# Kernel tuning notes

Measured on AMD Instinct MI355X. Metric: run time of the kernel, lower is better.

Reference implementation:

```python
import jax, jax.numpy as jnp
import numpy as np

B, T, D, N = 64, 32, 128, 128


def setup_inputs() -> dict:
    key = jax.random.key(0)
    ks = jax.random.split(key, 7)
    init_mu = 0.05
    ini_sigma = -4.6
    inp = {
        'x': jax.random.normal(ks[0], (B, T, D), dtype=jnp.float32),
        'U_z': init_mu * jax.random.normal(ks[1], (D, N), dtype=jnp.float32),
        'W_z': init_mu * jax.random.normal(ks[2], (N, N), dtype=jnp.float32),
        'U_r': init_mu * jax.random.normal(ks[3], (D, N), dtype=jnp.float32),
        'W_r': init_mu * jax.random.normal(ks[4], (N, N), dtype=jnp.float32),
        'U_h': init_mu * jax.random.normal(ks[5], (D, N), dtype=jnp.float32),
        'W_h': init_mu * jax.random.normal(ks[6], (N, N), dtype=jnp.float32),
        'uz_sigma': jnp.full((N,), ini_sigma, dtype=jnp.float32),
        'wz_sigma': jnp.full((N,), ini_sigma, dtype=jnp.float32),
        'ur_sigma': jnp.full((N,), ini_sigma, dtype=jnp.float32),
        'wr_sigma': jnp.full((N,), ini_sigma, dtype=jnp.float32),
        'uh_sigma': jnp.full((N,), ini_sigma, dtype=jnp.float32),
        'wh_sigma': jnp.full((N,), ini_sigma, dtype=jnp.float32),
    }
    return inp


def _outer(a, b):
    # [B,n] x [B,n] -> [B,n,n]
    return a[:, :, None] * b[:, None, :]


def _hadamard_sigma(s1, s2, m1, m2):
    # s1*s2 + diag(m1) s2 diag(m1) + diag(m2) s1 diag(m2)
    return s1 * s2 + _outer(m1, m1) * s2 + _outer(m2, m2) * s1


def reference(x, U_z, W_z, U_r, W_r, U_h, W_h,
              uz_sigma, wz_sigma, ur_sigma, wr_sigma, uh_sigma, wh_sigma):
    b, t, d = x.shape
    n = U_z.shape[1]
    idx = jnp.arange(n)
    sp = jax.nn.softplus
    dUz, dWz = jnp.diag(sp(uz_sigma)), jnp.diag(sp(wz_sigma))
    dUr, dWr = jnp.diag(sp(ur_sigma)), jnp.diag(sp(wr_sigma))
    dUh, dWh = jnp.diag(sp(uh_sigma)), jnp.diag(sp(wh_sigma))

    def step(carry, xt):
        mu_p, S_p = carry  # [B,n], [B,n,n]
        xx = jnp.sum(xt * xt, axis=1)[:, None, None]
        pp = jnp.sum(mu_p * mu_p, axis=1)[:, None, None]
        trS = jnp.trace(S_p, axis1=1, axis2=2)[:, None, None]

        def gate_cov(W, dW, dU):
            # W^T Sigma W + ||prev||^2 dW + tr(Sigma) dW + ||x||^2 dU
            S1 = jnp.einsum('ki,bkl,lj->bij', W, S_p, W)
            return S1 + pp * dW + trS * dW + xx * dU

        az = xt @ U_z + mu_p @ W_z
        z = jax.nn.sigmoid(az)
        gz = z * (1.0 - z)
        S_z = gate_cov(W_z, dWz, dUz) * _outer(gz, gz)

        ar = xt @ U_r + mu_p @ W_r
        r = jax.nn.sigmoid(ar)
        gr = r * (1.0 - r)
        S_r = gate_cov(W_r, dWr, dUr) * _outer(gr, gr)

        rh = mu_p * r
        ah = xt @ U_h + rh @ W_h
        h = jnp.tanh(ah)
        gh = 1.0 - h * h
        S_g = _hadamard_sigma(S_p, S_r, mu_p, r)
        rr = jnp.sum(rh * rh, axis=1)[:, None, None]
        trg = jnp.trace(S_g, axis1=1, axis2=2)[:, None, None]
        S_hh = jnp.einsum('ki,bkl,lj->bij', W_h, S_g, W_h) + rr * dWh + trg * dWh + xx * dUh
        S_h = S_hh * _outer(gh, gh)

        mu = z * mu_p + (1.0 - z) * h
        sa = _hadamard_sigma(S_z, S_p, z, mu_p)
        sb = _hadamard_sigma(S_z, S_h, 1.0 - z, h)
        S = sa + sb - S_z * _outer(mu_p, h) - S_z * _outer(h, mu_p)
        S = jnp.where(jnp.isfinite(S), S, jnp.zeros_like(S))
        S = S.at[:, idx, idx].set(jnp.abs(S[:, idx, idx]))
        return (mu, S), (mu, S)

    mu0 = jnp.zeros((b, n), dtype=x.dtype)
    S0 = jnp.zeros((b, n, n), dtype=x.dtype)
    _, (mu_seq, S_seq) = jax.lax.scan(step, (mu0, S0), jnp.swapaxes(x, 0, 1))
    # [B,T,n], [B,T,n,n]
    return jnp.swapaxes(mu_seq, 0, 1), jnp.swapaxes(S_seq, 0, 1)
```

## Files before the change

### kernel.cpp

```cpp
#include <hip/hip_runtime.h>
#include <math.h>

#define B_ 64
#define T_ 32
#define D_ 128
#define N_ 128
#define SBS 72
#define PTS 136

typedef __attribute__((ext_vector_type(8))) short s8v;
typedef __attribute__((ext_vector_type(4))) float f4;

__device__ __forceinline__ float softplus_f(float v){ return (v > 20.f) ? v : log1pf(expf(v)); }
__device__ __forceinline__ float sigmoid_f(float v){ return 1.f / (1.f + expf(-v)); }
__device__ __forceinline__ float wred(float v){
#pragma unroll
    for (int o = 32; o > 0; o >>= 1) v += __shfl_down(v, o, 64);
    return v;
}
__device__ __forceinline__ void split2(float v, unsigned short& h, unsigned short& l){
    unsigned int u  = __float_as_uint(v);
    unsigned int rh = u + 0x7fffu + ((u >> 16) & 1u);
    h = (unsigned short)(rh >> 16);
    float fh = __uint_as_float(rh & 0xffff0000u);
    float lo = v - fh;
    unsigned int ul = __float_as_uint(lo);
    unsigned int rl = ul + 0x7fffu + ((ul >> 16) & 1u);
    l = (unsigned short)(rl >> 16);
}
__device__ __forceinline__ void split4_store(float4 v, unsigned short* hp, unsigned short* lp){
    unsigned short h0,h1,h2,h3,l0,l1,l2,l3;
    split2(v.x,h0,l0); split2(v.y,h1,l1); split2(v.z,h2,l2); split2(v.w,h3,l3);
    uint2 H = make_uint2((unsigned)h0 | ((unsigned)h1 << 16), (unsigned)h2 | ((unsigned)h3 << 16));
    uint2 L = make_uint2((unsigned)l0 | ((unsigned)l1 << 16), (unsigned)l2 | ((unsigned)l3 << 16));
    *(uint2*)hp = H; *(uint2*)lp = L;
}
__device__ __forceinline__ f4 mfma3(s8v ah, s8v al, s8v bh, s8v bl, f4 c){
    c = __builtin_amdgcn_mfma_f32_16x16x32_bf16(ah, bh, c, 0, 0, 0);
    c = __builtin_amdgcn_mfma_f32_16x16x32_bf16(ah, bl, c, 0, 0, 0);
    c = __builtin_amdgcn_mfma_f32_16x16x32_bf16(al, bh, c, 0, 0, 0);
    return c;
}

__global__ __launch_bounds__(256)
void prep_w(const float* __restrict__ Wz, const float* __restrict__ Wr,
            const float* __restrict__ Wh, unsigned short* __restrict__ WT){
    int gate = blockIdx.x, n0 = blockIdx.y * 16, tid = threadIdx.x;
    const float* W = (gate == 0) ? Wz : (gate == 1) ? Wr : Wh;
    unsigned short* hi = WT + (size_t)gate * 32768;
    unsigned short* lo = hi + 16384;
#pragma unroll
    for (int e = 0; e < 8; ++e){
        int idx = tid + e * 256;
        int n = n0 + (idx >> 7), k = idx & 127;
        float v = W[(size_t)k * 128 + n];
        unsigned short h, l; split2(v, h, l);
        hi[(size_t)n * 128 + k] = h;
        lo[(size_t)n * 128 + k] = l;
    }
}

__global__ __launch_bounds__(256)
void prep_xu(const float* __restrict__ x, const float* __restrict__ Uz,
             const float* __restrict__ Ur, const float* __restrict__ Uh,
             float* __restrict__ XU, float* __restrict__ XX){
    int bt = blockIdx.x, tid = threadIdx.x;
    __shared__ float sX[128];
    __shared__ float sRed[256];
    __shared__ float sP[4];
    if (tid < 128) sX[tid] = x[(size_t)bt * 128 + tid];
    __syncthreads();
    {
        float v = (tid < 128) ? sX[tid] * sX[tid] : 0.f;
        v = wred(v);
        if ((tid & 63) == 0) sP[tid >> 6] = v;
    }
    const float* Us[3] = {Uz, Ur, Uh};
#pragma unroll 1
    for (int g = 0; g < 3; ++g){
        int n = tid & 127, hf = tid >> 7;
        float p = 0.f;
#pragma unroll 8
        for (int k = hf * 64; k < hf * 64 + 64; ++k) p = fmaf(sX[k], Us[g][(size_t)k * 128 + n], p);
        sRed[tid] = p;
        __syncthreads();
        if (tid < 128) XU[(size_t)g * (2048 * 128) + (size_t)bt * 128 + tid] = sRed[tid] + sRed[tid + 128];
        __syncthreads();
    }
    if (tid == 0) XX[bt] = sP[0] + sP[1] + sP[2] + sP[3];
}

__global__ __launch_bounds__(256, 1)
void step_zr(const float* __restrict__ Wz, const float* __restrict__ Wr, const float* __restrict__ Wh,
             const float* __restrict__ uzs, const float* __restrict__ wzs,
             const float* __restrict__ urs, const float* __restrict__ wrs,
             const unsigned short* __restrict__ WT,
             const float* __restrict__ XU, const float* __restrict__ XX,
             float* __restrict__ mu_out, const float* __restrict__ S_out,
             float* __restrict__ wsSz, float* __restrict__ wsSr,
             float* __restrict__ wsVec, int t)
{
    const int b = blockIdx.y, j0 = blockIdx.x * 32, tid = threadIdx.x;
    const int lane = tid & 63, w = tid >> 6, q = (tid >> 4) & 3, lm = tid & 15;

    __shared__ alignas(16) char sBig[36864];
    unsigned short* sShi = (unsigned short*)sBig;
    unsigned short* sSlo = (unsigned short*)(sBig + 128 * SBS * 2);
    unsigned short* sPT  = (unsigned short*)sBig;

    __shared__ float sMu[128], sZ[128], sGz[128], sR[128], sGr[128], sRh[128];
    __shared__ float sSP[4][128];
    __shared__ float sRed[256];
    __shared__ float sScalA[4], sScalB[4], sScalC[4];

    const int bt = b * T_ + t;
    const float* Sp = (t > 0) ? (S_out + (size_t)(bt - 1) * 16384) : S_out;

    if (tid < 128) sMu[tid] = (t > 0) ? mu_out[(size_t)(bt - 1) * 128 + tid] : 0.f;
    for (int a = tid; a < 512; a += 256){
        int tb = a >> 7, n = a & 127;
        const float* src = (tb == 0) ? uzs : (tb == 1) ? wzs : (tb == 2) ? urs : wrs;
        sSP[tb][n] = softplus_f(src[n]);
    }
    __syncthreads();

    {
        int g = tid >> 7, n = tid & 127;
        const float* Wg = g ? Wr : Wz;
        float a = XU[(size_t)g * (2048 * 128) + (size_t)bt * 128 + n];
#pragma unroll 16
        for (int k = 0; k < 128; ++k) a = fmaf(sMu[k], Wg[(size_t)k * 128 + n], a);
        float gg = sigmoid_f(a);
        if (!g){ sZ[n] = gg; sGz[n] = gg * (1.f - gg); }
        else   { sR[n] = gg; sGr[n] = gg * (1.f - gg); }
    }
    __syncthreads();

    if (tid < 128) sRh[tid] = sMu[tid] * sR[tid];
    {
        float v1 = (tid < 128) ? sMu[tid] * sMu[tid] : 0.f;
        float v2 = (tid < 128 && t > 0) ? Sp[(size_t)tid * 129] : 0.f;
        v1 = wred(v1); v2 = wred(v2);
        if (lane == 0){ sScalA[w] = v1; sScalB[w] = v2; }
    }
    __syncthreads();

    {
        int n = tid & 127, hf = tid >> 7;
        float p = 0.f;
#pragma unroll 16
        for (int k = hf * 64; k < hf * 64 + 64; ++k) p = fmaf(sRh[k], Wh[(size_t)k * 128 + n], p);
        sRed[tid] = p;
        float v = (tid < 128) ? sRh[tid] * sRh[tid] : 0.f;
        v = wred(v);
        if (lane == 0) sScalC[w] = v;
    }
    __syncthreads();

    if (tid < 128){
        float ah = XU[(size_t)2 * (2048 * 128) + (size_t)bt * 128 + tid] + sRed[tid] + sRed[tid + 128];
        float h = tanhf(ah);
        float z = sZ[tid];
        if (blockIdx.x == 0){
            mu_out[(size_t)bt * 128 + tid] = z * sMu[tid] + (1.f - z) * h;
            float* vbp = wsVec + (size_t)b * 520;
            vbp[tid] = z; vbp[128 + tid] = sR[tid]; vbp[256 + tid] = h; vbp[384 + tid] = 1.f - h * h;
            if (tid == 0) vbp[512] = sScalC[0] + sScalC[1] + sScalC[2] + sScalC[3];
        }
    }

    f4 accP[8];
#pragma unroll
    for (int i = 0; i < 8; ++i) accP[i] = (f4){0.f, 0.f, 0.f, 0.f};

    for (int half = 0; half < 2; ++half){
        __syncthreads();
        {
            int l0g = half * 64;
#pragma unroll
            for (int i = 0; i < 8; ++i){
                int idx4 = tid + i * 256;
                int row = idx4 >> 4, c4 = idx4 & 15;
                float4 v = make_float4(0.f, 0.f, 0.f, 0.f);
                if (t > 0) v = *(const float4*)(Sp + (size_t)row * 128 + l0g + c4 * 4);
                split4_store(v, &sShi[row * SBS + c4 * 4], &sSlo[row * SBS + c4 * 4]);
            }
        }
        __syncthreads();
#pragma unroll
        for (int c = 0; c < 2; ++c){
            int lloc = c * 32 + q * 8;
            int lglob = half * 64 + lloc;
            s8v aH[2], aL[2];
#pragma unroll
            for (int s = 0; s < 2; ++s){
                int row = (w * 2 + s) * 16 + lm;
                aH[s] = *(const s8v*)&sShi[row * SBS + lloc];
                aL[s] = *(const s8v*)&sSlo[row * SBS + lloc];
            }
#pragma unroll
            for (int nt = 0; nt < 2; ++nt){
                size_t off = (size_t)(j0 + nt * 16 + lm) * 128 + lglob;
                s8v bzH = *(const s8v*)&WT[off];
                s8v bzL = *(const s8v*)&WT[16384 + off];
                s8v brH = *(const s8v*)&WT[32768 + off];
                s8v brL = *(const s8v*)&WT[49152 + off];
#pragma unroll
                for (int s = 0; s < 2; ++s){
                    accP[s * 2 + nt]     = mfma3(aH[s], aL[s], bzH, bzL, accP[s * 2 + nt]);
                    accP[4 + s * 2 + nt] = mfma3(aH[s], aL[s], brH, brL, accP[4 + s * 2 + nt]);
                }
            }
        }
    }
    __syncthreads();

#pragma unroll
    for (int g = 0; g < 2; ++g)
#pragma unroll
        for (int s = 0; s < 2; ++s)
#pragma unroll
            for (int nt = 0; nt < 2; ++nt){
                f4 a = accP[g * 4 + s * 2 + nt];
                int kb = (w * 2 + s) * 16 + q * 4;
                int jr = nt * 16 + lm;
                split4_store(make_float4(a[0], a[1], a[2], a[3]),
                             &sPT[(g * 2 + 0) * (32 * PTS) + jr * PTS + kb],
                             &sPT[(g * 2 + 1) * (32 * PTS) + jr * PTS + kb]);
            }
    __syncthreads();

    float pp  = sScalA[0] + sScalA[1] + sScalA[2] + sScalA[3];
    float trS = sScalB[0] + sScalB[1] + sScalB[2] + sScalB[3];
    float pt  = pp + trS;
    float xxv = XX[bt];

#pragma unroll 1
    for (int g = 0; g < 2; ++g){
        const unsigned short* AH = WT + (size_t)g * 32768;
        const unsigned short* AL = AH + 16384;
        const unsigned short* PH = sPT + (g * 2) * (32 * PTS);
        const unsigned short* PL = PH + (32 * PTS);
        f4 acc[4];
#pragma unroll
        for (int i = 0; i < 4; ++i) acc[i] = (f4){0.f, 0.f, 0.f, 0.f};
#pragma unroll
        for (int c = 0; c < 4; ++c){
            int k0 = c * 32 + q * 8;
            s8v aH[2], aL[2];
#pragma unroll
            for (int s = 0; s < 2; ++s){
                size_t row = (size_t)((w * 2 + s) * 16 + lm) * 128 + k0;
                aH[s] = *(const s8v*)&AH[row];
                aL[s] = *(const s8v*)&AL[row];
            }
#pragma unroll
            for (int nt = 0; nt < 2; ++nt){
                int jj = (nt * 16 + lm) * PTS + k0;
                s8v bH = *(const s8v*)&PH[jj];
                s8v bL = *(const s8v*)&PL[jj];
#pragma unroll
                for (int s = 0; s < 2; ++s)
                    acc[s * 2 + nt] = mfma3(aH[s], aL[s], bH, bL, acc[s * 2 + nt]);
            }
        }
        const float* G   = g ? sGr : sGz;
        const float* spU = g ? sSP[2] : sSP[0];
        const float* spW = g ? sSP[3] : sSP[1];
        float* dst = (g ? wsSr : wsSz) + (size_t)b * 16384;
#pragma unroll
        for (int s = 0; s < 2; ++s)
#pragma unroll
            for (int nt = 0; nt < 2; ++nt){
                f4 a = acc[s * 2 + nt];
                int ib = (w * 2 + s) * 16 + q * 4;
                int j = j0 + nt * 16 + lm;
                float gj = G[j];
#pragma unroll
                for (int r = 0; r < 4; ++r){
                    int i = ib + r;
                    float v = a[r];
                    if (i == j) v += pt * spW[i] + xxv * spU[i];
                    dst[(size_t)i * 128 + j] = v * G[i] * gj;
                }
            }
    }
}

__global__ __launch_bounds__(256, 1)
void step_h(const float* __restrict__ uhs, const float* __restrict__ whs,
            const unsigned short* __restrict__ WT,
            const float* __restrict__ XX,
            const float* __restrict__ mu_out, float* __restrict__ S_out,
            const float* __restrict__ wsSz, const float* __restrict__ wsSr,
            const float* __restrict__ wsVec, int t)
{
    const int b = blockIdx.y, j0 = blockIdx.x * 32, tid = threadIdx.x;
    const int lane = tid & 63, w = tid >> 6, q = (tid >> 4) & 3, lm = tid & 15;

    __shared__ alignas(16) char sBig[36864];
    unsigned short* sGhi = (unsigned short*)sBig;
    unsigned short* sGlo = (unsigned short*)(sBig + 128 * SBS * 2);
    unsigned short* sPT  = (unsigned short*)sBig;

    __shared__ float sMu[128], sZ[128], sR[128], sH[128], sGh[128];
    __shared__ float sSPu[128], sSPw[128];
    __shared__ float sScal[4];

    const int bt = b * T_ + t;
    const float* Sp = (t > 0) ? (S_out + (size_t)(bt - 1) * 16384) : S_out;
    const float* Sr = wsSr + (size_t)b * 16384;
    const float* vb = wsVec + (size_t)b * 520;
    const unsigned short* WTH = WT + 65536;
    const unsigned short* WTL = WT + 81920;

    if (tid < 128){
        sZ[tid] = vb[tid]; sR[tid] = vb[128 + tid]; sH[tid] = vb[256 + tid]; sGh[tid] = vb[384 + tid];
        sMu[tid] = (t > 0) ? mu_out[(size_t)(bt - 1) * 128 + tid] : 0.f;
        sSPu[tid] = softplus_f(uhs[tid]); sSPw[tid] = softplus_f(whs[tid]);
    }

    f4 accP[4];
#pragma unroll
    for (int i = 0; i < 4; ++i) accP[i] = (f4){0.f, 0.f, 0.f, 0.f};
    float tdiag = 0.f;

    for (int half = 0; half < 2; ++half){
        __syncthreads();
        {
            int l0g = half * 64;
#pragma unroll
            for (int i = 0; i < 8; ++i){
                int idx4 = tid + i * 256;
                int row = idx4 >> 4, c4 = idx4 & 15;
                int colg = l0g + c4 * 4;
                float4 sp4 = make_float4(0.f, 0.f, 0.f, 0.f);
                if (t > 0) sp4 = *(const float4*)(Sp + (size_t)row * 128 + colg);
                float4 sr4 = *(const float4*)(Sr + (size_t)row * 128 + colg);
                float muk = sMu[row], rk = sR[row];
                float4 mc = *(const float4*)&sMu[colg];
                float4 rc = *(const float4*)&sR[colg];
                float4 gv;
                gv.x = sp4.x * sr4.x + muk * mc.x * sr4.x + rk * rc.x * sp4.x;
                gv.y = sp4.y * sr4.y + muk * mc.y * sr4.y + rk * rc.y * sp4.y;
                gv.z = sp4.z * sr4.z + muk * mc.z * sr4.z + rk * rc.z * sp4.z;
                gv.w = sp4.w * sr4.w + muk * mc.w * sr4.w + rk * rc.w * sp4.w;
                int d = row - colg;
                if (d >= 0 && d < 4) tdiag += (d == 0) ? gv.x : (d == 1) ? gv.y : (d == 2) ? gv.z : gv.w;
                split4_store(gv, &sGhi[row * SBS + c4 * 4], &sGlo[row * SBS + c4 * 4]);
            }
        }
        __syncthreads();
#pragma unroll
        for (int c = 0; c < 2; ++c){
            int lloc = c * 32 + q * 8;
            int lglob = half * 64 + lloc;
            s8v aH[2], aL[2];
#pragma unroll
            for (int s = 0; s < 2; ++s){
                int row = (w * 2 + s) * 16 + lm;
                aH[s] = *(const s8v*)&sGhi[row * SBS + lloc];
                aL[s] = *(const s8v*)&sGlo[row * SBS + lloc];
            }
#pragma unroll
            for (int nt = 0; nt < 2; ++nt){
                size_t off = (size_t)(j0 + nt * 16 + lm) * 128 + lglob;
                s8v bH = *(const s8v*)&WTH[off];
                s8v bL = *(const s8v*)&WTL[off];
#pragma unroll
                for (int s = 0; s < 2; ++s)
                    accP[s * 2 + nt] = mfma3(aH[s], aL[s], bH, bL, accP[s * 2 + nt]);
            }
        }
    }
    float td = wred(tdiag);
    __syncthreads();
    if (lane == 0) sScal[w] = td;
#pragma unroll
    for (int s = 0; s < 2; ++s)
#pragma unroll
        for (int nt = 0; nt < 2; ++nt){
            f4 a = accP[s * 2 + nt];
            int kb = (w * 2 + s) * 16 + q * 4;
            int jr = nt * 16 + lm;
            split4_store(make_float4(a[0], a[1], a[2], a[3]),
                         &sPT[jr * PTS + kb],
                         &sPT[(32 * PTS) + jr * PTS + kb]);
        }
    __syncthreads();

    f4 acc[4];
#pragma unroll
    for (int i = 0; i < 4; ++i) acc[i] = (f4){0.f, 0.f, 0.f, 0.f};
#pragma unroll
    for (int c = 0; c < 4; ++c){
        int k0 = c * 32 + q * 8;
        s8v aH[2], aL[2];
#pragma unroll
        for (int s = 0; s < 2; ++s){
            size_t row = (size_t)((w * 2 + s) * 16 + lm) * 128 + k0;
            aH[s] = *(const s8v*)&WTH[row];
            aL[s] = *(const s8v*)&WTL[row];
        }
#pragma unroll
        for (int nt = 0; nt < 2; ++nt){
            int jj = (nt * 16 + lm) * PTS + k0;
            s8v bH = *(const s8v*)&sPT[jj];
            s8v bL = *(const s8v*)&sPT[(32 * PTS) + jj];
#pragma unroll
            for (int s = 0; s < 2; ++s)
                acc[s * 2 + nt] = mfma3(aH[s], aL[s], bH, bL, acc[s * 2 + nt]);
        }
    }

    float trg  = sScal[0] + sScal[1] + sScal[2] + sScal[3];
    float coef = vb[512] + trg;
    float xxv  = XX[bt];
    const float* Szb = wsSz + (size_t)b * 16384;
    float* outS = S_out + (size_t)bt * 16384;
#pragma unroll
    for (int s = 0; s < 2; ++s)
#pragma unroll
        for (int nt = 0; nt < 2; ++nt){
            f4 a = acc[s * 2 + nt];
            int ib = (w * 2 + s) * 16 + q * 4;
            int j = j0 + nt * 16 + lm;
            float zj = sZ[j], ghj = sGh[j];
#pragma unroll
            for (int r = 0; r < 4; ++r){
                int i = ib + r;
                float shh = a[r];
                if (i == j) shh += coef * sSPw[i] + xxv * sSPu[i];
                float sh = shh * sGh[i] * ghj;
                float szv = Szb[(size_t)i * 128 + j];
                float spv = (t > 0) ? Sp[(size_t)i * 128 + j] : 0.f;
                float dmi = sMu[i] - sH[i], dmj = sMu[j] - sH[j];
                float zi = sZ[i];
                float sv = szv * (spv + sh + dmi * dmj) + zi * zj * spv + (1.f - zi) * (1.f - zj) * sh;
                if (!isfinite(sv)) sv = 0.f;
                if (i == j) sv = fabsf(sv);
                outS[(size_t)i * 128 + j] = sv;
            }
        }
}

extern "C" void kernel_launch(void* const* d_in, const int* in_sizes, int n_in,
                              void* d_out, int out_size, void* d_ws, size_t ws_size,
                              hipStream_t stream)
{
    (void)in_sizes; (void)n_in; (void)out_size; (void)ws_size;
    const float* x   = (const float*)d_in[0];
    const float* Uz  = (const float*)d_in[1];
    const float* Wz  = (const float*)d_in[2];
    const float* Ur  = (const float*)d_in[3];
    const float* Wr  = (const float*)d_in[4];
    const float* Uh  = (const float*)d_in[5];
    const float* Wh  = (const float*)d_in[6];
    const float* uzs = (const float*)d_in[7];
    const float* wzs = (const float*)d_in[8];
    const float* urs = (const float*)d_in[9];
    const float* wrs = (const float*)d_in[10];
    const float* uhs = (const float*)d_in[11];
    const float* whs = (const float*)d_in[12];

    float* mu_out = (float*)d_out;
    float* S_out  = (float*)d_out + (size_t)B_ * T_ * N_;

    char* ws = (char*)d_ws;
    unsigned short* wsWT = (unsigned short*)ws;
    float* wsXU  = (float*)(ws + 196608);
    float* wsXX  = (float*)(ws + 3342336);
    float* wsSz  = (float*)(ws + 3350528);
    float* wsSr  = (float*)(ws + 7544832);
    float* wsVec = (float*)(ws + 11739136);

    hipLaunchKernelGGL(prep_w, dim3(3, 8), dim3(256), 0, stream, Wz, Wr, Wh, wsWT);
    hipLaunchKernelGGL(prep_xu, dim3(2048), dim3(256), 0, stream, x, Uz, Ur, Uh, wsXU, wsXX);

    dim3 grid(4, B_), blk(256);
    for (int t = 0; t < T_; ++t){
        hipLaunchKernelGGL(step_zr, grid, blk, 0, stream,
                           Wz, Wr, Wh, uzs, wzs, urs, wrs,
                           wsWT, wsXU, wsXX, mu_out, S_out, wsSz, wsSr, wsVec, t);
        hipLaunchKernelGGL(step_h, grid, blk, 0, stream,
                           uhs, whs, wsWT, wsXX, mu_out, S_out, wsSz, wsSr, wsVec, t);
    }
}
```

Before: 1.678 ms.

## Fuse all timesteps into one persistent per-batch kernel with covariance held in LDS

Replaces the 64 per-timestep launches (step_zr and step_h, each on a 4x64 grid) with a single kernel: one 1024-thread block per batch element loops over all 32 timesteps. The previous covariance and mu stay in shared memory, so the kernel no longer re-reads S_prev from global memory or round-trips S_z, S_r and the gate vectors through workspace buffers. The intent is to remove launch overhead and global-memory traffic between steps. In exchange, only 64 blocks run, one per batch element and each using most of a CU's LDS, which lowers GPU-wide parallelism and adds many block-wide barriers per step.

```diff
diff --git a/kernel.cpp b/kernel.cpp
--- a/kernel.cpp
+++ b/kernel.cpp
@@ -5,8 +5,7 @@
 #define T_ 32
 #define D_ 128
 #define N_ 128
-#define SBS 72
-#define PTS 136
+#define ST 136
 
 typedef __attribute__((ext_vector_type(8))) short s8v;
 typedef __attribute__((ext_vector_type(4))) float f4;
@@ -90,117 +89,119 @@
     if (tid == 0) XX[bt] = sP[0] + sP[1] + sP[2] + sP[3];
 }
 
-__global__ __launch_bounds__(256, 1)
-void step_zr(const float* __restrict__ Wz, const float* __restrict__ Wr, const float* __restrict__ Wh,
-             const float* __restrict__ uzs, const float* __restrict__ wzs,
-             const float* __restrict__ urs, const float* __restrict__ wrs,
-             const unsigned short* __restrict__ WT,
-             const float* __restrict__ XU, const float* __restrict__ XX,
-             float* __restrict__ mu_out, const float* __restrict__ S_out,
-             float* __restrict__ wsSz, float* __restrict__ wsSr,
-             float* __restrict__ wsVec, int t)
+__global__ __launch_bounds__(1024)
+void gru_fused(const float* __restrict__ Wz, const float* __restrict__ Wr,
+               const float* __restrict__ Wh,
+               const unsigned short* __restrict__ WT,
+               const float* __restrict__ XU, const float* __restrict__ XX,
+               const float* __restrict__ uzs, const float* __restrict__ wzs,
+               const float* __restrict__ urs, const float* __restrict__ wrs,
+               const float* __restrict__ uhs, const float* __restrict__ whs,
+               float* __restrict__ mu_out, float* __restrict__ S_out)
 {
-    const int b = blockIdx.y, j0 = blockIdx.x * 32, tid = threadIdx.x;
-    const int lane = tid & 63, w = tid >> 6, q = (tid >> 4) & 3, lm = tid & 15;
-
-    __shared__ alignas(16) char sBig[36864];
-    unsigned short* sShi = (unsigned short*)sBig;
-    unsigned short* sSlo = (unsigned short*)(sBig + 128 * SBS * 2);
-    unsigned short* sPT  = (unsigned short*)sBig;
-
-    __shared__ float sMu[128], sZ[128], sGz[128], sR[128], sGr[128], sRh[128];
-    __shared__ float sSP[4][128];
-    __shared__ float sRed[256];
-    __shared__ float sScalA[4], sScalB[4], sScalC[4];
-
-    const int bt = b * T_ + t;
-    const float* Sp = (t > 0) ? (S_out + (size_t)(bt - 1) * 16384) : S_out;
-
-    if (tid < 128) sMu[tid] = (t > 0) ? mu_out[(size_t)(bt - 1) * 128 + tid] : 0.f;
-    for (int a = tid; a < 512; a += 256){
-        int tb = a >> 7, n = a & 127;
-        const float* src = (tb == 0) ? uzs : (tb == 1) ? wzs : (tb == 2) ? urs : wrs;
-        sSP[tb][n] = softplus_f(src[n]);
+    const int b = blockIdx.x, tid = threadIdx.x;
+    const int w16 = tid >> 6, g4 = w16 >> 2, wl = w16 & 3;
+    const int q = (tid >> 4) & 3, lm = tid & 15;
+
+    __shared__ alignas(16) float sS[128 * 128];
+    __shared__ alignas(16) unsigned short sRegion[2 * 128 * ST];
+    __shared__ float sMuB[2][128];
+    __shared__ float sZ[128], sGz[128], sR[128], sGr[128], sRh[128], sH[128], sGh[128];
+    __shared__ float sSP[6][128];
+    __shared__ float sRed[1024];
+    __shared__ float sScalTd[16];
+    __shared__ float sScalP[2], sScalQ[2];
+    __shared__ float sPt, sRR;
+
+    unsigned short* sHi = sRegion;
+    unsigned short* sLo = sRegion + 128 * ST;
+
+    for (int i = tid; i < 128 * 128; i += 1024) sS[i] = 0.f;
+    for (int i = tid; i < 2 * 128 * ST; i += 1024) sRegion[i] = 0;
+    if (tid < 768){
+        int tb = tid >> 7, n = tid & 127;
+        const float* srcs[6] = {uzs, wzs, urs, wrs, uhs, whs};
+        sSP[tb][n] = softplus_f(srcs[tb][n]);
     }
+    if (tid < 128) sMuB[0][tid] = 0.f;
     __syncthreads();
 
-    {
-        int g = tid >> 7, n = tid & 127;
-        const float* Wg = g ? Wr : Wz;
-        float a = XU[(size_t)g * (2048 * 128) + (size_t)bt * 128 + n];
-#pragma unroll 16
-        for (int k = 0; k < 128; ++k) a = fmaf(sMu[k], Wg[(size_t)k * 128 + n], a);
-        float gg = sigmoid_f(a);
-        if (!g){ sZ[n] = gg; sGz[n] = gg * (1.f - gg); }
-        else   { sR[n] = gg; sGr[n] = gg * (1.f - gg); }
-    }
-    __syncthreads();
-
-    if (tid < 128) sRh[tid] = sMu[tid] * sR[tid];
-    {
-        float v1 = (tid < 128) ? sMu[tid] * sMu[tid] : 0.f;
-        float v2 = (tid < 128 && t > 0) ? Sp[(size_t)tid * 129] : 0.f;
-        v1 = wred(v1); v2 = wred(v2);
-        if (lane == 0){ sScalA[w] = v1; sScalB[w] = v2; }
-    }
-    __syncthreads();
-
-    {
-        int n = tid & 127, hf = tid >> 7;
-        float p = 0.f;
-#pragma unroll 16
-        for (int k = hf * 64; k < hf * 64 + 64; ++k) p = fmaf(sRh[k], Wh[(size_t)k * 128 + n], p);
-        sRed[tid] = p;
-        float v = (tid < 128) ? sRh[tid] * sRh[tid] : 0.f;
-        v = wred(v);
-        if (lane == 0) sScalC[w] = v;
-    }
-    __syncthreads();
-
-    if (tid < 128){
-        float ah = XU[(size_t)2 * (2048 * 128) + (size_t)bt * 128 + tid] + sRed[tid] + sRed[tid + 128];
-        float h = tanhf(ah);
-        float z = sZ[tid];
-        if (blockIdx.x == 0){
-            mu_out[(size_t)bt * 128 + tid] = z * sMu[tid] + (1.f - z) * h;
-            float* vbp = wsVec + (size_t)b * 520;
-            vbp[tid] = z; vbp[128 + tid] = sR[tid]; vbp[256 + tid] = h; vbp[384 + tid] = 1.f - h * h;
-            if (tid == 0) vbp[512] = sScalC[0] + sScalC[1] + sScalC[2] + sScalC[3];
-        }
-    }
-
-    f4 accP[8];
-#pragma unroll
-    for (int i = 0; i < 8; ++i) accP[i] = (f4){0.f, 0.f, 0.f, 0.f};
-
-    for (int half = 0; half < 2; ++half){
-        __syncthreads();
+    for (int t = 0; t < T_; ++t){
+        const int bt = b * T_ + t;
+        const float* muP = sMuB[t & 1];
+        float* muN = sMuB[(t + 1) & 1];
+        const float xxv = XX[bt];
+
+        float xuzr = 0.f, xuh = 0.f;
+        if (tid < 256) xuzr = XU[(size_t)(tid >> 7) * (2048 * 128) + (size_t)bt * 128 + (tid & 127)];
+        if (tid < 128) xuh = XU[(size_t)2 * (2048 * 128) + (size_t)bt * 128 + tid];
+
         {
-            int l0g = half * 64;
-#pragma unroll
-            for (int i = 0; i < 8; ++i){
-                int idx4 = tid + i * 256;
-                int row = idx4 >> 4, c4 = idx4 & 15;
-                float4 v = make_float4(0.f, 0.f, 0.f, 0.f);
-                if (t > 0) v = *(const float4*)(Sp + (size_t)row * 128 + l0g + c4 * 4);
-                split4_store(v, &sShi[row * SBS + c4 * 4], &sSlo[row * SBS + c4 * 4]);
-            }
-        }
-        __syncthreads();
-#pragma unroll
-        for (int c = 0; c < 2; ++c){
-            int lloc = c * 32 + q * 8;
-            int lglob = half * 64 + lloc;
+            int n = tid & 127, kq = (tid >> 7) & 3, g = tid >> 9;
+            const float* Wg = g ? Wr : Wz;
+            float p = 0.f;
+#pragma unroll 8
+            for (int k = kq * 32; k < kq * 32 + 32; ++k) p = fmaf(muP[k], Wg[(size_t)k * 128 + n], p);
+            sRed[tid] = p;
+        }
+        __syncthreads();
+
+        if (tid < 256){
+            int g = tid >> 7, n = tid & 127, base = g * 512 + n;
+            float a = xuzr
+                    + sRed[base] + sRed[base + 128] + sRed[base + 256] + sRed[base + 384];
+            float gg = sigmoid_f(a);
+            if (!g){ sZ[n] = gg; sGz[n] = gg * (1.f - gg); }
+            else   { sR[n] = gg; sGr[n] = gg * (1.f - gg); sRh[n] = muP[n] * gg; }
+        }
+        __syncthreads();
+
+        if (tid < 512){
+            int n = tid & 127, kq = tid >> 7;
+            float p = 0.f;
+#pragma unroll 8
+            for (int k = kq * 32; k < kq * 32 + 32; ++k) p = fmaf(sRh[k], Wh[(size_t)k * 128 + n], p);
+            sRed[tid] = p;
+        } else if (tid < 640){
+            int n = tid & 127;
+            float v = muP[n] * muP[n] + sS[n * 129];
+            v = wred(v);
+            if ((tid & 63) == 0) sScalP[(tid >> 6) & 1] = v;
+        } else if (tid < 768){
+            int n = tid & 127;
+            float v = sRh[n] * sRh[n];
+            v = wred(v);
+            if ((tid & 63) == 0) sScalQ[(tid >> 6) & 1] = v;
+        }
+        __syncthreads();
+
+        if (tid < 128){
+            float ah = xuh + sRed[tid] + sRed[tid + 128] + sRed[tid + 256] + sRed[tid + 384];
+            float h = tanhf(ah);
+            float z = sZ[tid];
+            sH[tid] = h; sGh[tid] = 1.f - h * h;
+            float m = z * muP[tid] + (1.f - z) * h;
+            muN[tid] = m;
+            mu_out[(size_t)bt * 128 + tid] = m;
+        } else if (tid == 128){ sPt = sScalP[0] + sScalP[1]; }
+        else if (tid == 129){ sRR = sScalQ[0] + sScalQ[1]; }
+
+        f4 accP[8];
+#pragma unroll
+        for (int i = 0; i < 8; ++i) accP[i] = (f4){0.f, 0.f, 0.f, 0.f};
+#pragma unroll
+        for (int c = 0; c < 4; ++c){
+            int k0 = c * 32 + q * 8;
             s8v aH[2], aL[2];
 #pragma unroll
             for (int s = 0; s < 2; ++s){
-                int row = (w * 2 + s) * 16 + lm;
-                aH[s] = *(const s8v*)&sShi[row * SBS + lloc];
-                aL[s] = *(const s8v*)&sSlo[row * SBS + lloc];
-            }
-#pragma unroll
-            for (int nt = 0; nt < 2; ++nt){
-                size_t off = (size_t)(j0 + nt * 16 + lm) * 128 + lglob;
+                int row = (wl * 2 + s) * 16 + lm;
+                aH[s] = *(const s8v*)&sHi[row * ST + k0];
+                aL[s] = *(const s8v*)&sLo[row * ST + k0];
+            }
+#pragma unroll
+            for (int nt = 0; nt < 2; ++nt){
+                size_t off = (size_t)(g4 * 32 + nt * 16 + lm) * 128 + k0;
                 s8v bzH = *(const s8v*)&WT[off];
                 s8v bzL = *(const s8v*)&WT[16384 + off];
                 s8v brH = *(const s8v*)&WT[32768 + off];
@@ -212,236 +213,233 @@
                 }
             }
         }
-    }
-    __syncthreads();
-
-#pragma unroll
-    for (int g = 0; g < 2; ++g)
+        __syncthreads();
+
 #pragma unroll
         for (int s = 0; s < 2; ++s)
 #pragma unroll
-            for (int nt = 0; nt < 2; ++nt){
-                f4 a = accP[g * 4 + s * 2 + nt];
-                int kb = (w * 2 + s) * 16 + q * 4;
-                int jr = nt * 16 + lm;
-                split4_store(make_float4(a[0], a[1], a[2], a[3]),
-                             &sPT[(g * 2 + 0) * (32 * PTS) + jr * PTS + kb],
-                             &sPT[(g * 2 + 1) * (32 * PTS) + jr * PTS + kb]);
-            }
-    __syncthreads();
-
-    float pp  = sScalA[0] + sScalA[1] + sScalA[2] + sScalA[3];
-    float trS = sScalB[0] + sScalB[1] + sScalB[2] + sScalB[3];
-    float pt  = pp + trS;
-    float xxv = XX[bt];
-
-#pragma unroll 1
-    for (int g = 0; g < 2; ++g){
-        const unsigned short* AH = WT + (size_t)g * 32768;
-        const unsigned short* AL = AH + 16384;
-        const unsigned short* PH = sPT + (g * 2) * (32 * PTS);
-        const unsigned short* PL = PH + (32 * PTS);
-        f4 acc[4];
-#pragma unroll
-        for (int i = 0; i < 4; ++i) acc[i] = (f4){0.f, 0.f, 0.f, 0.f};
+        for (int nt = 0; nt < 2; ++nt){
+            f4 a = accP[s * 2 + nt];
+            int kb = wl * 32 + s * 16 + q * 4;
+            int jr = g4 * 32 + nt * 16 + lm;
+            split4_store(make_float4(a[0], a[1], a[2], a[3]),
+                         &sHi[jr * ST + kb], &sLo[jr * ST + kb]);
+        }
+        __syncthreads();
+
+        float szc[16];
+        {
+            f4 acc[4];
+#pragma unroll
+            for (int i = 0; i < 4; ++i) acc[i] = (f4){0.f, 0.f, 0.f, 0.f};
+#pragma unroll
+            for (int c = 0; c < 4; ++c){
+                int k0 = c * 32 + q * 8;
+                s8v aH[2], aL[2];
+#pragma unroll
+                for (int s = 0; s < 2; ++s){
+                    size_t row = (size_t)((g4 * 2 + s) * 16 + lm) * 128 + k0;
+                    aH[s] = *(const s8v*)&WT[row];
+                    aL[s] = *(const s8v*)&WT[16384 + row];
+                }
+#pragma unroll
+                for (int nt = 0; nt < 2; ++nt){
+                    int j = (wl * 2 + nt) * 16 + lm;
+                    s8v bH = *(const s8v*)&sHi[j * ST + k0];
+                    s8v bL = *(const s8v*)&sLo[j * ST + k0];
+#pragma unroll
+                    for (int s = 0; s < 2; ++s)
+                        acc[s * 2 + nt] = mfma3(aH[s], aL[s], bH, bL, acc[s * 2 + nt]);
+                }
+            }
+            float pt = sPt;
+#pragma unroll
+            for (int s = 0; s < 2; ++s)
+#pragma unroll
+            for (int nt = 0; nt < 2; ++nt){
+                f4 a = acc[s * 2 + nt];
+                int ib = g4 * 32 + s * 16 + q * 4;
+                int j  = wl * 32 + nt * 16 + lm;
+                float gj = sGz[j];
+#pragma unroll
+                for (int r = 0; r < 4; ++r){
+                    int i = ib + r;
+                    float v = a[r];
+                    if (i == j) v += pt * sSP[1][i] + xxv * sSP[0][i];
+                    szc[s * 8 + nt * 4 + r] = v * sGz[i] * gj;
+                }
+            }
+        }
+        __syncthreads();
+
+#pragma unroll
+        for (int s = 0; s < 2; ++s)
+#pragma unroll
+        for (int nt = 0; nt < 2; ++nt){
+            f4 a = accP[4 + s * 2 + nt];
+            int kb = wl * 32 + s * 16 + q * 4;
+            int jr = g4 * 32 + nt * 16 + lm;
+            split4_store(make_float4(a[0], a[1], a[2], a[3]),
+                         &sHi[jr * ST + kb], &sLo[jr * ST + kb]);
+        }
+        __syncthreads();
+
+        f4 accR[4];
+#pragma unroll
+        for (int i = 0; i < 4; ++i) accR[i] = (f4){0.f, 0.f, 0.f, 0.f};
 #pragma unroll
         for (int c = 0; c < 4; ++c){
             int k0 = c * 32 + q * 8;
             s8v aH[2], aL[2];
 #pragma unroll
             for (int s = 0; s < 2; ++s){
-                size_t row = (size_t)((w * 2 + s) * 16 + lm) * 128 + k0;
-                aH[s] = *(const s8v*)&AH[row];
-                aL[s] = *(const s8v*)&AL[row];
-            }
-#pragma unroll
-            for (int nt = 0; nt < 2; ++nt){
-                int jj = (nt * 16 + lm) * PTS + k0;
-                s8v bH = *(const s8v*)&PH[jj];
-                s8v bL = *(const s8v*)&PL[jj];
+                size_t row = (size_t)((g4 * 2 + s) * 16 + lm) * 128 + k0;
+                aH[s] = *(const s8v*)&WT[32768 + row];
+                aL[s] = *(const s8v*)&WT[49152 + row];
+            }
+#pragma unroll
+            for (int nt = 0; nt < 2; ++nt){
+                int j = (wl * 2 + nt) * 16 + lm;
+                s8v bH = *(const s8v*)&sHi[j * ST + k0];
+                s8v bL = *(const s8v*)&sLo[j * ST + k0];
 #pragma unroll
                 for (int s = 0; s < 2; ++s)
-                    acc[s * 2 + nt] = mfma3(aH[s], aL[s], bH, bL, acc[s * 2 + nt]);
-            }
-        }
-        const float* G   = g ? sGr : sGz;
-        const float* spU = g ? sSP[2] : sSP[0];
-        const float* spW = g ? sSP[3] : sSP[1];
-        float* dst = (g ? wsSr : wsSz) + (size_t)b * 16384;
-#pragma unroll
-        for (int s = 0; s < 2; ++s)
-#pragma unroll
-            for (int nt = 0; nt < 2; ++nt){
-                f4 a = acc[s * 2 + nt];
-                int ib = (w * 2 + s) * 16 + q * 4;
-                int j = j0 + nt * 16 + lm;
-                float gj = G[j];
+                    accR[s * 2 + nt] = mfma3(aH[s], aL[s], bH, bL, accR[s * 2 + nt]);
+            }
+        }
+        __syncthreads();
+
+        {
+            float pt = sPt;
+            float td = 0.f;
+#pragma unroll
+            for (int s = 0; s < 2; ++s)
+#pragma unroll
+            for (int nt = 0; nt < 2; ++nt){
+                f4 a = accR[s * 2 + nt];
+                int ib = g4 * 32 + s * 16 + q * 4;
+                int j  = wl * 32 + nt * 16 + lm;
+                float gj = sGr[j], muj = muP[j], rj = sR[j];
+                float sg[4];
 #pragma unroll
                 for (int r = 0; r < 4; ++r){
                     int i = ib + r;
                     float v = a[r];
-                    if (i == j) v += pt * spW[i] + xxv * spU[i];
-                    dst[(size_t)i * 128 + j] = v * G[i] * gj;
-                }
-            }
+                    if (i == j) v += pt * sSP[3][i] + xxv * sSP[2][i];
+                    float srv = v * sGr[i] * gj;
+                    float spv = sS[i * 128 + j];
+                    float gv = spv * srv + muP[i] * muj * srv + sR[i] * rj * spv;
+                    if (i == j) td += gv;
+                    sg[r] = gv;
+                }
+                split4_store(make_float4(sg[0], sg[1], sg[2], sg[3]),
+                             &sHi[j * ST + ib], &sLo[j * ST + ib]);
+            }
+            td = wred(td);
+            if ((tid & 63) == 0) sScalTd[w16] = td;
+        }
+        __syncthreads();
+
+        f4 accH[4];
+#pragma unroll
+        for (int i = 0; i < 4; ++i) accH[i] = (f4){0.f, 0.f, 0.f, 0.f};
+#pragma unroll
+        for (int c = 0; c < 4; ++c){
+            int k0 = c * 32 + q * 8;
+            s8v aH[2], aL[2];
+#pragma unroll
+            for (int s = 0; s < 2; ++s){
+                int row = (wl * 2 + s) * 16 + lm;
+                aH[s] = *(const s8v*)&sHi[row * ST + k0];
+                aL[s] = *(const s8v*)&sLo[row * ST + k0];
+            }
+#pragma unroll
+            for (int nt = 0; nt < 2; ++nt){
+                size_t off = (size_t)(g4 * 32 + nt * 16 + lm) * 128 + k0;
+                s8v bH = *(const s8v*)&WT[65536 + off];
+                s8v bL = *(const s8v*)&WT[81920 + off];
+#pragma unroll
+                for (int s = 0; s < 2; ++s)
+                    accH[s * 2 + nt] = mfma3(aH[s], aL[s], bH, bL, accH[s * 2 + nt]);
+            }
+        }
+        __syncthreads();
+
+#pragma unroll
+        for (int s = 0; s < 2; ++s)
+#pragma unroll
+        for (int nt = 0; nt < 2; ++nt){
+            f4 a = accH[s * 2 + nt];
+            int kb = wl * 32 + s * 16 + q * 4;
+            int jr = g4 * 32 + nt * 16 + lm;
+            split4_store(make_float4(a[0], a[1], a[2], a[3]),
+                         &sHi[jr * ST + kb], &sLo[jr * ST + kb]);
+        }
+        __syncthreads();
+
+        f4 accC[4];
+#pragma unroll
+        for (int i = 0; i < 4; ++i) accC[i] = (f4){0.f, 0.f, 0.f, 0.f};
+#pragma unroll
+        for (int c = 0; c < 4; ++c){
+            int k0 = c * 32 + q * 8;
+            s8v aH[2], aL[2];
+#pragma unroll
+            for (int s = 0; s < 2; ++s){
+                size_t row = (size_t)((g4 * 2 + s) * 16 + lm) * 128 + k0;
+                aH[s] = *(const s8v*)&WT[65536 + row];
+                aL[s] = *(const s8v*)&WT[81920 + row];
+            }
+#pragma unroll
+            for (int nt = 0; nt < 2; ++nt){
+                int j = (wl * 2 + nt) * 16 + lm;
+                s8v bH = *(const s8v*)&sHi[j * ST + k0];
+                s8v bL = *(const s8v*)&sLo[j * ST + k0];
+#pragma unroll
+                for (int s = 0; s < 2; ++s)
+                    accC[s * 2 + nt] = mfma3(aH[s], aL[s], bH, bL, accC[s * 2 + nt]);
+            }
+        }
+        __syncthreads();
+
+        {
+            float trg = 0.f;
+#pragma unroll
+            for (int k = 0; k < 16; ++k) trg += sScalTd[k];
+            float coef = sRR + trg;
+            float* outS = S_out + (size_t)bt * 16384;
+#pragma unroll
+            for (int s = 0; s < 2; ++s)
+#pragma unroll
+            for (int nt = 0; nt < 2; ++nt){
+                f4 a = accC[s * 2 + nt];
+                int ib = g4 * 32 + s * 16 + q * 4;
+                int j  = wl * 32 + nt * 16 + lm;
+                float zj = sZ[j], ghj = sGh[j], dmj = muP[j] - sH[j];
+                float sv4[4];
+#pragma unroll
+                for (int r = 0; r < 4; ++r){
+                    int i = ib + r;
+                    float shh = a[r];
+                    if (i == j) shh += coef * sSP[5][i] + xxv * sSP[4][i];
+                    float sh = shh * sGh[i] * ghj;
+                    float szv = szc[s * 8 + nt * 4 + r];
+                    float spv = sS[i * 128 + j];
+                    float dmi = muP[i] - sH[i];
+                    float zi = sZ[i];
+                    float sv = szv * (spv + sh + dmi * dmj) + zi * zj * spv + (1.f - zi) * (1.f - zj) * sh;
+                    if (!isfinite(sv)) sv = 0.f;
+                    if (i == j) sv = fabsf(sv);
+                    sS[i * 128 + j] = sv;
+                    outS[(size_t)i * 128 + j] = sv;
+                    sv4[r] = sv;
+                }
+                split4_store(make_float4(sv4[0], sv4[1], sv4[2], sv4[3]),
+                             &sHi[j * ST + ib], &sLo[j * ST + ib]);
+            }
+        }
+        __syncthreads();
     }
-}
-
-__global__ __launch_bounds__(256, 1)
-void step_h(const float* __restrict__ uhs, const float* __restrict__ whs,
-            const unsigned short* __restrict__ WT,
-            const float* __restrict__ XX,
-            const float* __restrict__ mu_out, float* __restrict__ S_out,
-            const float* __restrict__ wsSz, const float* __restrict__ wsSr,
-            const float* __restrict__ wsVec, int t)
-{
-    const int b = blockIdx.y, j0 = blockIdx.x * 32, tid = threadIdx.x;
-    const int lane = tid & 63, w = tid >> 6, q = (tid >> 4) & 3, lm = tid & 15;
-
-    __shared__ alignas(16) char sBig[36864];
-    unsigned short* sGhi = (unsigned short*)sBig;
-    unsigned short* sGlo = (unsigned short*)(sBig + 128 * SBS * 2);
-    unsigned short* sPT  = (unsigned short*)sBig;
-
-    __shared__ float sMu[128], sZ[128], sR[128], sH[128], sGh[128];
-    __shared__ float sSPu[128], sSPw[128];
-    __shared__ float sScal[4];
-
-    const int bt = b * T_ + t;
-    const float* Sp = (t > 0) ? (S_out + (size_t)(bt - 1) * 16384) : S_out;
-    const float* Sr = wsSr + (size_t)b * 16384;
-    const float* vb = wsVec + (size_t)b * 520;
-    const unsigned short* WTH = WT + 65536;
-    const unsigned short* WTL = WT + 81920;
-
-    if (tid < 128){
-        sZ[tid] = vb[tid]; sR[tid] = vb[128 + tid]; sH[tid] = vb[256 + tid]; sGh[tid] = vb[384 + tid];
-        sMu[tid] = (t > 0) ? mu_out[(size_t)(bt - 1) * 128 + tid] : 0.f;
-        sSPu[tid] = softplus_f(uhs[tid]); sSPw[tid] = softplus_f(whs[tid]);
-    }
-
-    f4 accP[4];
-#pragma unroll
-    for (int i = 0; i < 4; ++i) accP[i] = (f4){0.f, 0.f, 0.f, 0.f};
-    float tdiag = 0.f;
-
-    for (int half = 0; half < 2; ++half){
-        __syncthreads();
-        {
-            int l0g = half * 64;
-#pragma unroll
-            for (int i = 0; i < 8; ++i){
-                int idx4 = tid + i * 256;
-                int row = idx4 >> 4, c4 = idx4 & 15;
-                int colg = l0g + c4 * 4;
-                float4 sp4 = make_float4(0.f, 0.f, 0.f, 0.f);
-                if (t > 0) sp4 = *(const float4*)(Sp + (size_t)row * 128 + colg);
-                float4 sr4 = *(const float4*)(Sr + (size_t)row * 128 + colg);
-                float muk = sMu[row], rk = sR[row];
-                float4 mc = *(const float4*)&sMu[colg];
-                float4 rc = *(const float4*)&sR[colg];
-                float4 gv;
-                gv.x = sp4.x * sr4.x + muk * mc.x * sr4.x + rk * rc.x * sp4.x;
-                gv.y = sp4.y * sr4.y + muk * mc.y * sr4.y + rk * rc.y * sp4.y;
-                gv.z = sp4.z * sr4.z + muk * mc.z * sr4.z + rk * rc.z * sp4.z;
-                gv.w = sp4.w * sr4.w + muk * mc.w * sr4.w + rk * rc.w * sp4.w;
-                int d = row - colg;
-                if (d >= 0 && d < 4) tdiag += (d == 0) ? gv.x : (d == 1) ? gv.y : (d == 2) ? gv.z : gv.w;
-                split4_store(gv, &sGhi[row * SBS + c4 * 4], &sGlo[row * SBS + c4 * 4]);
-            }
-        }
-        __syncthreads();
-#pragma unroll
-        for (int c = 0; c < 2; ++c){
-            int lloc = c * 32 + q * 8;
-            int lglob = half * 64 + lloc;
-            s8v aH[2], aL[2];
-#pragma unroll
-            for (int s = 0; s < 2; ++s){
-                int row = (w * 2 + s) * 16 + lm;
-                aH[s] = *(const s8v*)&sGhi[row * SBS + lloc];
-                aL[s] = *(const s8v*)&sGlo[row * SBS + lloc];
-            }
-#pragma unroll
-            for (int nt = 0; nt < 2; ++nt){
-                size_t off = (size_t)(j0 + nt * 16 + lm) * 128 + lglob;
-                s8v bH = *(const s8v*)&WTH[off];
-                s8v bL = *(const s8v*)&WTL[off];
-#pragma unroll
-                for (int s = 0; s < 2; ++s)
-                    accP[s * 2 + nt] = mfma3(aH[s], aL[s], bH, bL, accP[s * 2 + nt]);
-            }
-        }
-    }
-    float td = wred(tdiag);
-    __syncthreads();
-    if (lane == 0) sScal[w] = td;
-#pragma unroll
-    for (int s = 0; s < 2; ++s)
-#pragma unroll
-        for (int nt = 0; nt < 2; ++nt){
-            f4 a = accP[s * 2 + nt];
-            int kb = (w * 2 + s) * 16 + q * 4;
-            int jr = nt * 16 + lm;
-            split4_store(make_float4(a[0], a[1], a[2], a[3]),
-                         &sPT[jr * PTS + kb],
-                         &sPT[(32 * PTS) + jr * PTS + kb]);
-        }
-    __syncthreads();
-
-    f4 acc[4];
-#pragma unroll
-    for (int i = 0; i < 4; ++i) acc[i] = (f4){0.f, 0.f, 0.f, 0.f};
-#pragma unroll
-    for (int c = 0; c < 4; ++c){
-        int k0 = c * 32 + q * 8;
-        s8v aH[2], aL[2];
-#pragma unroll
-        for (int s = 0; s < 2; ++s){
-            size_t row = (size_t)((w * 2 + s) * 16 + lm) * 128 + k0;
-            aH[s] = *(const s8v*)&WTH[row];
-            aL[s] = *(const s8v*)&WTL[row];
-        }
-#pragma unroll
-        for (int nt = 0; nt < 2; ++nt){
-            int jj = (nt * 16 + lm) * PTS + k0;
-            s8v bH = *(const s8v*)&sPT[jj];
-            s8v bL = *(const s8v*)&sPT[(32 * PTS) + jj];
-#pragma unroll
-            for (int s = 0; s < 2; ++s)
-                acc[s * 2 + nt] = mfma3(aH[s], aL[s], bH, bL, acc[s * 2 + nt]);
-        }
-    }
-
-    float trg  = sScal[0] + sScal[1] + sScal[2] + sScal[3];
-    float coef = vb[512] + trg;
-    float xxv  = XX[bt];
-    const float* Szb = wsSz + (size_t)b * 16384;
-    float* outS = S_out + (size_t)bt * 16384;
-#pragma unroll
-    for (int s = 0; s < 2; ++s)
-#pragma unroll
-        for (int nt = 0; nt < 2; ++nt){
-            f4 a = acc[s * 2 + nt];
-            int ib = (w * 2 + s) * 16 + q * 4;
-            int j = j0 + nt * 16 + lm;
-            float zj = sZ[j], ghj = sGh[j];
-#pragma unroll
-            for (int r = 0; r < 4; ++r){
-                int i = ib + r;
-                float shh = a[r];
-                if (i == j) shh += coef * sSPw[i] + xxv * sSPu[i];
-                float sh = shh * sGh[i] * ghj;
-                float szv = Szb[(size_t)i * 128 + j];
-                float spv = (t > 0) ? Sp[(size_t)i * 128 + j] : 0.f;
-                float dmi = sMu[i] - sH[i], dmj = sMu[j] - sH[j];
-                float zi = sZ[i];
-                float sv = szv * (spv + sh + dmi * dmj) + zi * zj * spv + (1.f - zi) * (1.f - zj) * sh;
-                if (!isfinite(sv)) sv = 0.f;
-                if (i == j) sv = fabsf(sv);
-                outS[(size_t)i * 128 + j] = sv;
-            }
-        }
 }
 
 extern "C" void kernel_launch(void* const* d_in, const int* in_sizes, int n_in,
@@ -470,19 +468,10 @@
     unsigned short* wsWT = (unsigned short*)ws;
     float* wsXU  = (float*)(ws + 196608);
     float* wsXX  = (float*)(ws + 3342336);
-    float* wsSz  = (float*)(ws + 3350528);
-    float* wsSr  = (float*)(ws + 7544832);
-    float* wsVec = (float*)(ws + 11739136);
 
     hipLaunchKernelGGL(prep_w, dim3(3, 8), dim3(256), 0, stream, Wz, Wr, Wh, wsWT);
     hipLaunchKernelGGL(prep_xu, dim3(2048), dim3(256), 0, stream, x, Uz, Ur, Uh, wsXU, wsXX);
-
-    dim3 grid(4, B_), blk(256);
-    for (int t = 0; t < T_; ++t){
-        hipLaunchKernelGGL(step_zr, grid, blk, 0, stream,
-                           Wz, Wr, Wh, uzs, wzs, urs, wrs,
-                           wsWT, wsXU, wsXX, mu_out, S_out, wsSz, wsSr, wsVec, t);
-        hipLaunchKernelGGL(step_h, grid, blk, 0, stream,
-                           uhs, whs, wsWT, wsXX, mu_out, S_out, wsSz, wsSr, wsVec, t);
-    }
-}
+    hipLaunchKernelGGL(gru_fused, dim3(B_), dim3(1024), 0, stream,
+                       Wz, Wr, Wh, wsWT, wsXU, wsXX,
+                       uzs, wzs, urs, wrs, uhs, whs, mu_out, S_out);
+}
```

New measurement: 2.481 ms. 47.9% more time.
